# Performance work log

Hardware: AMD Instinct MI355X
Metric: run time of the kernel (lower is better)

Reference implementation:

```python
import jax, jax.numpy as jnp
import numpy as np

B, C, E = 4, 2048, 1024
H, D = 16, 64

def setup_inputs() -> dict:
    key = jax.random.key(0)
    kx, kq, kk, kv, ko = jax.random.split(key, 5)
    s = 1.0 / np.sqrt(E)
    return {
        "x": jax.random.normal(kx, (B, C, E), dtype=jnp.float32),
        "W_q": jax.random.uniform(kq, (E, H * D), jnp.float32, -s, s),
        "W_k": jax.random.uniform(kk, (E, H * D), jnp.float32, -s, s),
        "W_v": jax.random.uniform(kv, (E, H * D), jnp.float32, -s, s),
        "W_o": jax.random.uniform(ko, (H * D, E), jnp.float32, -s, s),
    }

def reference(x, W_q, W_k, W_v, W_o):
    b, c, e = x.shape
    # project and split heads: [B, H, C, D]
    q = (x @ W_q).reshape(b, c, H, D).transpose(0, 2, 1, 3)
    k = (x @ W_k).reshape(b, c, H, D).transpose(0, 2, 1, 3)
    v = (x @ W_v).reshape(b, c, H, D).transpose(0, 2, 1, 3)
    scores = jnp.einsum('bhqd,bhkd->bhqk', q, k) / jnp.sqrt(jnp.float32(D))
    causal = jnp.tril(jnp.ones((c, c), dtype=bool))
    scores = jnp.where(causal, scores, -jnp.inf)
    weights = jax.nn.softmax(scores, axis=-1)
    hidden = jnp.einsum('bhqk,bhkd->bhqd', weights, v)
    hidden = hidden.transpose(0, 2, 1, 3).reshape(b, c, H * D)
    return hidden @ W_o
```

## Files before the change

kernel.cpp:

```cpp
#include <hip/hip_runtime.h>
#include <hip/hip_bf16.h>


typedef __attribute__((ext_vector_type(8))) short short8;
typedef __attribute__((ext_vector_type(4))) float floatx4;
typedef __attribute__((ext_vector_type(4))) unsigned short ushort4v;

__device__ __forceinline__ unsigned short f2bf(float f) {
    __hip_bfloat16 h = __float2bfloat16(f);
    return __builtin_bit_cast(unsigned short, h);
}

__device__ __forceinline__ void gl2lds16(const unsigned short* g, unsigned short* l) {
    __builtin_amdgcn_global_load_lds(
        (const __attribute__((address_space(1))) unsigned int*)g,
        (__attribute__((address_space(3))) unsigned int*)l, 16, 0, 0);
}

__global__ __launch_bounds__(256) void prep_kernel(const float* __restrict__ x,
                                                   const float* __restrict__ W0,
                                                   const float* __restrict__ W1,
                                                   const float* __restrict__ W2,
                                                   const float* __restrict__ W3,
                                                   unsigned short* __restrict__ xb,
                                                   unsigned short* __restrict__ wt) {
    __shared__ float tile[64][65];
    const int id = blockIdx.x;
    if (id < 8192) {
        const int i = id * 256 + threadIdx.x;
        const float4 v = ((const float4*)x)[i];
        ushort4v o;
        o[0] = f2bf(v.x); o[1] = f2bf(v.y); o[2] = f2bf(v.z); o[3] = f2bf(v.w);
        ((ushort4v*)xb)[i] = o;
        return;
    }
    const int t2 = id - 8192;
    const int z = t2 >> 8;
    const float* src = (z == 0) ? W0 : (z == 1) ? W1 : (z == 2) ? W2 : W3;
    const float scale = (z == 0) ? 0.18033688011112042f : 1.0f;
    unsigned short* dst = wt + (size_t)z * 1048576;
    const int k0 = ((t2 >> 4) & 15) * 64, n0 = (t2 & 15) * 64;
    const int t = threadIdx.x;
    const int r = t >> 4, c4 = (t & 15) * 4;
    #pragma unroll
    for (int p = 0; p < 4; ++p) {
        const int kk = p * 16 + r;
        const float4 v = *(const float4*)&src[(size_t)(k0 + kk) * 1024 + n0 + c4];
        tile[kk][c4 + 0] = v.x; tile[kk][c4 + 1] = v.y;
        tile[kk][c4 + 2] = v.z; tile[kk][c4 + 3] = v.w;
    }
    __syncthreads();
    #pragma unroll
    for (int p = 0; p < 4; ++p) {
        const int nn = p * 16 + r;
        ushort4v o;
        #pragma unroll
        for (int j = 0; j < 4; ++j) o[j] = f2bf(tile[c4 + j][nn] * scale);
        *(ushort4v*)&dst[(size_t)(n0 + nn) * 1024 + k0 + c4] = o;
    }
}

template<int MODE, int NBLK>
__global__ __launch_bounds__(256) void gemm128(const unsigned short* __restrict__ A,
                                               const unsigned short* __restrict__ Bt,
                                               unsigned short* __restrict__ obf,
                                               float* __restrict__ ofp) {
    constexpr int Kd = 1024;
    __shared__ __align__(16) unsigned short Al[128 * 64];
    __shared__ __align__(16) unsigned short Bl[128 * 64];
    const int id = blockIdx.x;
    const int xcd = id & 7;
    const int q = id >> 3;
    const int m_blk = xcd * 8 + (q & 7);
    const int n_blk = q >> 3;
    const int m0 = m_blk * 128, n0 = n_blk * 128;

    const int tid = threadIdx.x;
    const int lane = tid & 63, w = tid >> 6;
    const int quad = lane >> 4, l15 = lane & 15;
    const int wm = (w & 1) * 64, wn = (w >> 1) * 64;
    const int srow = lane >> 3, sc = lane & 7;
    const int gc = (sc ^ srow) * 8;

    floatx4 acc[4][4];
    #pragma unroll
    for (int i = 0; i < 4; ++i)
        #pragma unroll
        for (int j = 0; j < 4; ++j) acc[i][j] = (floatx4){0.f, 0.f, 0.f, 0.f};

    for (int kt = 0; kt < Kd / 64; ++kt) {
        const int k0 = kt * 64;
        #pragma unroll
        for (int p = 0; p < 4; ++p) {
            const int row0 = w * 32 + p * 8;
            gl2lds16(&A[(size_t)(m0 + row0 + srow) * Kd + k0 + gc], &Al[row0 * 64]);
            gl2lds16(&Bt[(size_t)(n0 + row0 + srow) * Kd + k0 + gc], &Bl[row0 * 64]);
        }
        __syncthreads();
        #pragma unroll
        for (int kk = 0; kk < 2; ++kk) {
            short8 af[4], bfv[4];
            #pragma unroll
            for (int i = 0; i < 4; ++i) {
                const int row = wm + i * 16 + l15;
                af[i] = *(const short8*)&Al[row * 64 + ((kk * 4 + quad) ^ (row & 7)) * 8];
            }
            #pragma unroll
            for (int i = 0; i < 4; ++i) {
                const int row = wn + i * 16 + l15;
                bfv[i] = *(const short8*)&Bl[row * 64 + ((kk * 4 + quad) ^ (row & 7)) * 8];
            }
            #pragma unroll
            for (int i = 0; i < 4; ++i)
                #pragma unroll
                for (int j = 0; j < 4; ++j)
                    acc[i][j] = __builtin_amdgcn_mfma_f32_16x16x32_bf16(
                        af[i], bfv[j], acc[i][j], 0, 0, 0);
        }
        __syncthreads();
    }

    #pragma unroll
    for (int i = 0; i < 4; ++i) {
        if (MODE == 0 && n0 >= 2048) {
            #pragma unroll
            for (int j = 0; j < 4; ++j) {
                const int mb = m0 + wm + i * 16 + quad * 4;
                const int n = n0 + wn + j * 16 + l15;
                const int b = mb >> 11, c0 = mb & 2047;
                const int nl = n & 1023, hh = nl >> 6, d = nl & 63;
                ushort4v pv;
                #pragma unroll
                for (int r = 0; r < 4; ++r) pv[r] = f2bf(acc[i][j][r]);
                *(ushort4v*)&obf[16777216 + ((size_t)(b * 16 + hh) * 64 + d) * 2048 + c0] = pv;
            }
        } else {
            #pragma unroll
            for (int r = 0; r < 4; ++r) {
                const int m = m0 + wm + i * 16 + quad * 4 + r;
                #pragma unroll
                for (int j = 0; j < 4; ++j) {
                    const int n = n0 + wn + j * 16 + l15;
                    const float v = acc[i][j][r];
                    if (MODE == 0) {
                        const int b = m >> 11, c = m & 2047;
                        const int z = n >> 10, nl = n & 1023, hh = nl >> 6, d = nl & 63;
                        obf[(size_t)z * 8388608 +
                            ((size_t)(b * 16 + hh) * 2048 + c) * 64 + d] = f2bf(v);
                    } else {
                        ofp[(size_t)m * 1024 + n] = v;
                    }
                }
            }
        }
    }
}

__global__ __launch_bounds__(512, 8) void attn_kernel(const unsigned short* __restrict__ Q,
                                                      const unsigned short* __restrict__ K,
                                                      const unsigned short* __restrict__ Vt,
                                                      unsigned short* __restrict__ Hid) {
    __shared__ __align__(16) unsigned short Kl[64 * 64];
    __shared__ __align__(16) unsigned short Vl[64 * 64];
    __shared__ __align__(16) unsigned short Pl[8][16 * 72];
    const int id = blockIdx.x;
    const int bh = (id >> 7) * 8 + (id & 7);
    const int qt = 15 - ((id >> 3) & 15);
    const int b = bh >> 4, h = bh & 15;
    const int tid = threadIdx.x, w = tid >> 6, lane = tid & 63;
    const int quad = lane >> 4, l15 = lane & 15;
    const int sw = quad ^ (l15 & 7);
    const int srow = lane >> 3, sc = lane & 7;
    const int g8 = (sc ^ srow) * 8;
    const size_t bhs = (size_t)(b * 16 + h) * 2048 * 64;
    const unsigned short* Qb = Q + bhs;
    const unsigned short* Kb = K + bhs;
    const unsigned short* Vb = Vt + bhs;

    const int q0 = qt * 128;
    const int qw = q0 + w * 16;
    const int myq = qw + l15;
    const short8 bq0 = *(const short8*)&Qb[(size_t)myq * 64 + quad * 8];
    const short8 bq1 = *(const short8*)&Qb[(size_t)myq * 64 + 32 + quad * 8];

    floatx4 o[4];
    #pragma unroll
    for (int i = 0; i < 4; ++i) o[i] = (floatx4){0.f, 0.f, 0.f, 0.f};
    float li = 0.f;

    const int nT = (q0 + 128) >> 6;
    for (int t = 0; t < nT; ++t) {
        const int k0 = t * 64;
        {
            const int krow = w * 8 + srow;
            gl2lds16(&Kb[(size_t)(k0 + krow) * 64 + g8], &Kl[w * 512]);
            gl2lds16(&Vb[(size_t)krow * 2048 + k0 + g8], &Vl[w * 512]);
        }
        __syncthreads();
        if (k0 <= qw + 15) {
            floatx4 s[4];
            #pragma unroll
            for (int kf = 0; kf < 4; ++kf) {
                const int row = kf * 16 + l15;
                const short8 ka0 = *(const short8*)&Kl[row * 64 + sw * 8];
                const short8 ka1 = *(const short8*)&Kl[row * 64 + (sw ^ 4) * 8];
                floatx4 ss = (floatx4){0.f, 0.f, 0.f, 0.f};
                ss = __builtin_amdgcn_mfma_f32_16x16x32_bf16(ka0, bq0, ss, 0, 0, 0);
                ss = __builtin_amdgcn_mfma_f32_16x16x32_bf16(ka1, bq1, ss, 0, 0, 0);
                s[kf] = ss;
            }
            if (k0 + 63 > qw) {
                #pragma unroll
                for (int kf = 0; kf < 4; ++kf) {
                    ushort4v pw;
                    #pragma unroll
                    for (int r = 0; r < 4; ++r) {
                        const int key = k0 + kf * 16 + quad * 4 + r;
                        const float p = (key > myq) ? 0.f
                                        : __builtin_amdgcn_exp2f(s[kf][r]);
                        li += p;
                        pw[r] = f2bf(p);
                    }
                    *(ushort4v*)&Pl[w][l15 * 72 + kf * 16 + quad * 4] = pw;
                }
            } else {
                #pragma unroll
                for (int kf = 0; kf < 4; ++kf) {
                    ushort4v pw;
                    #pragma unroll
                    for (int r = 0; r < 4; ++r) {
                        const float p = __builtin_amdgcn_exp2f(s[kf][r]);
                        li += p;
                        pw[r] = f2bf(p);
                    }
                    *(ushort4v*)&Pl[w][l15 * 72 + kf * 16 + quad * 4] = pw;
                }
            }
            __threadfence_block();
            const short8 pb0 = *(const short8*)&Pl[w][l15 * 72 + quad * 8];
            const short8 pb1 = *(const short8*)&Pl[w][l15 * 72 + 32 + quad * 8];
            #pragma unroll
            for (int nt = 0; nt < 4; ++nt) {
                const int row = nt * 16 + l15;
                const short8 va0 = *(const short8*)&Vl[row * 64 + sw * 8];
                const short8 va1 = *(const short8*)&Vl[row * 64 + (sw ^ 4) * 8];
                floatx4 oo = o[nt];
                oo = __builtin_amdgcn_mfma_f32_16x16x32_bf16(va0, pb0, oo, 0, 0, 0);
                oo = __builtin_amdgcn_mfma_f32_16x16x32_bf16(va1, pb1, oo, 0, 0, 0);
                o[nt] = oo;
            }
        }
        __syncthreads();
    }

    li += __shfl_xor(li, 16, 64);
    li += __shfl_xor(li, 32, 64);
    const float inv = 1.f / li;
    #pragma unroll
    for (int nt = 0; nt < 4; ++nt) {
        ushort4v ov;
        #pragma unroll
        for (int r = 0; r < 4; ++r) ov[r] = f2bf(o[nt][r] * inv);
        *(ushort4v*)&Hid[((size_t)b * 2048 + myq) * 1024 + h * 64 + nt * 16 + quad * 4] = ov;
    }
}

extern "C" void kernel_launch(void* const* d_in, const int* in_sizes, int n_in,
                              void* d_out, int out_size, void* d_ws, size_t ws_size,
                              hipStream_t stream) {
    const float* x  = (const float*)d_in[0];
    const float* Wq = (const float*)d_in[1];
    const float* Wk = (const float*)d_in[2];
    const float* Wv = (const float*)d_in[3];
    const float* Wo = (const float*)d_in[4];
    float* out = (float*)d_out;
    unsigned short* ws = (unsigned short*)d_ws;

    const size_t XB  = 0;
    const size_t WQT = 8388608;
    const size_t QO  = 12582912;
    const size_t HO  = 37748736;

    prep_kernel<<<9216, 256, 0, stream>>>(x, Wq, Wk, Wv, Wo, ws + XB, ws + WQT);

    gemm128<0, 24><<<1536, 256, 0, stream>>>(ws + XB, ws + WQT, ws + QO, nullptr);
    attn_kernel<<<1024, 512, 0, stream>>>(ws + QO, ws + QO + 8388608,
                                          ws + QO + 16777216, ws + HO);
    gemm128<1, 8><<<512, 256, 0, stream>>>(ws + HO, ws + WQT + 3145728, nullptr, out);
}
```

Before: 262.7 us.

## Double-buffer K/V tiles and pair causal query tiles per attention block

The attention kernel now double-buffers K and V tiles in shared memory, so the next tile's global-to-LDS load is issued before the current tile is computed, and one barrier per iteration is removed. Each block also handles two query tiles, xq and 15-xq, so every block gets the same causal work and the grid is halved to 512 blocks. The aim is to hide load latency and balance work across blocks. In exchange, LDS use doubles and the occupancy hint in launch_bounds is dropped, which may lower occupancy, and the smaller grid may leave compute units idle.

```diff
diff --git a/kernel.cpp b/kernel.cpp
--- a/kernel.cpp
+++ b/kernel.cpp
@@ -156,112 +156,121 @@
     }
 }
 
-__global__ __launch_bounds__(512, 8) void attn_kernel(const unsigned short* __restrict__ Q,
-                                                      const unsigned short* __restrict__ K,
-                                                      const unsigned short* __restrict__ Vt,
-                                                      unsigned short* __restrict__ Hid) {
-    __shared__ __align__(16) unsigned short Kl[64 * 64];
-    __shared__ __align__(16) unsigned short Vl[64 * 64];
+__global__ __launch_bounds__(512) void attn_kernel(const unsigned short* __restrict__ Q,
+                                                   const unsigned short* __restrict__ K,
+                                                   const unsigned short* __restrict__ Vt,
+                                                   unsigned short* __restrict__ Hid) {
+    __shared__ __align__(16) unsigned short Kl[2][64 * 64];
+    __shared__ __align__(16) unsigned short Vl[2][64 * 64];
     __shared__ __align__(16) unsigned short Pl[8][16 * 72];
     const int id = blockIdx.x;
-    const int bh = (id >> 7) * 8 + (id & 7);
-    const int qt = 15 - ((id >> 3) & 15);
+    const int bh = (id >> 6) * 8 + (id & 7);
+    const int xq = (id >> 3) & 7;
     const int b = bh >> 4, h = bh & 15;
     const int tid = threadIdx.x, w = tid >> 6, lane = tid & 63;
     const int quad = lane >> 4, l15 = lane & 15;
     const int sw = quad ^ (l15 & 7);
     const int srow = lane >> 3, sc = lane & 7;
     const int g8 = (sc ^ srow) * 8;
+    const int krow = w * 8 + srow;
     const size_t bhs = (size_t)(b * 16 + h) * 2048 * 64;
     const unsigned short* Qb = Q + bhs;
     const unsigned short* Kb = K + bhs;
     const unsigned short* Vb = Vt + bhs;
 
-    const int q0 = qt * 128;
-    const int qw = q0 + w * 16;
-    const int myq = qw + l15;
-    const short8 bq0 = *(const short8*)&Qb[(size_t)myq * 64 + quad * 8];
-    const short8 bq1 = *(const short8*)&Qb[(size_t)myq * 64 + 32 + quad * 8];
-
-    floatx4 o[4];
-    #pragma unroll
-    for (int i = 0; i < 4; ++i) o[i] = (floatx4){0.f, 0.f, 0.f, 0.f};
-    float li = 0.f;
-
-    const int nT = (q0 + 128) >> 6;
-    for (int t = 0; t < nT; ++t) {
-        const int k0 = t * 64;
-        {
-            const int krow = w * 8 + srow;
-            gl2lds16(&Kb[(size_t)(k0 + krow) * 64 + g8], &Kl[w * 512]);
-            gl2lds16(&Vb[(size_t)krow * 2048 + k0 + g8], &Vl[w * 512]);
-        }
+    #pragma unroll
+    for (int pass = 0; pass < 2; ++pass) {
+        const int qt = pass ? (15 - xq) : xq;
+        const int q0 = qt * 128;
+        const int qw = q0 + w * 16;
+        const int myq = qw + l15;
+        const short8 bq0 = *(const short8*)&Qb[(size_t)myq * 64 + quad * 8];
+        const short8 bq1 = *(const short8*)&Qb[(size_t)myq * 64 + 32 + quad * 8];
+
+        floatx4 o[4];
+        #pragma unroll
+        for (int i = 0; i < 4; ++i) o[i] = (floatx4){0.f, 0.f, 0.f, 0.f};
+        float li = 0.f;
+
+        const int nT = (q0 + 128) >> 6;
         __syncthreads();
-        if (k0 <= qw + 15) {
-            floatx4 s[4];
-            #pragma unroll
-            for (int kf = 0; kf < 4; ++kf) {
-                const int row = kf * 16 + l15;
-                const short8 ka0 = *(const short8*)&Kl[row * 64 + sw * 8];
-                const short8 ka1 = *(const short8*)&Kl[row * 64 + (sw ^ 4) * 8];
-                floatx4 ss = (floatx4){0.f, 0.f, 0.f, 0.f};
-                ss = __builtin_amdgcn_mfma_f32_16x16x32_bf16(ka0, bq0, ss, 0, 0, 0);
-                ss = __builtin_amdgcn_mfma_f32_16x16x32_bf16(ka1, bq1, ss, 0, 0, 0);
-                s[kf] = ss;
-            }
-            if (k0 + 63 > qw) {
+        gl2lds16(&Kb[(size_t)krow * 64 + g8], &Kl[0][w * 512]);
+        gl2lds16(&Vb[(size_t)krow * 2048 + g8], &Vl[0][w * 512]);
+
+        for (int t = 0; t < nT; ++t) {
+            const int k0 = t * 64;
+            const int cb = t & 1;
+            __syncthreads();
+            if (t + 1 < nT) {
+                const int kn = k0 + 64;
+                gl2lds16(&Kb[(size_t)(kn + krow) * 64 + g8], &Kl[cb ^ 1][w * 512]);
+                gl2lds16(&Vb[(size_t)krow * 2048 + kn + g8], &Vl[cb ^ 1][w * 512]);
+            }
+            if (k0 <= qw + 15) {
+                floatx4 s[4];
                 #pragma unroll
                 for (int kf = 0; kf < 4; ++kf) {
-                    ushort4v pw;
+                    const int row = kf * 16 + l15;
+                    const short8 ka0 = *(const short8*)&Kl[cb][row * 64 + sw * 8];
+                    const short8 ka1 = *(const short8*)&Kl[cb][row * 64 + (sw ^ 4) * 8];
+                    floatx4 ss = (floatx4){0.f, 0.f, 0.f, 0.f};
+                    ss = __builtin_amdgcn_mfma_f32_16x16x32_bf16(ka0, bq0, ss, 0, 0, 0);
+                    ss = __builtin_amdgcn_mfma_f32_16x16x32_bf16(ka1, bq1, ss, 0, 0, 0);
+                    s[kf] = ss;
+                }
+                if (k0 + 63 > qw) {
                     #pragma unroll
-                    for (int r = 0; r < 4; ++r) {
-                        const int key = k0 + kf * 16 + quad * 4 + r;
-                        const float p = (key > myq) ? 0.f
-                                        : __builtin_amdgcn_exp2f(s[kf][r]);
-                        li += p;
-                        pw[r] = f2bf(p);
+                    for (int kf = 0; kf < 4; ++kf) {
+                        ushort4v pw;
+                        #pragma unroll
+                        for (int r = 0; r < 4; ++r) {
+                            const int key = k0 + kf * 16 + quad * 4 + r;
+                            const float p = (key > myq) ? 0.f
+                                            : __builtin_amdgcn_exp2f(s[kf][r]);
+                            li += p;
+                            pw[r] = f2bf(p);
+                        }
+                        *(ushort4v*)&Pl[w][l15 * 72 + kf * 16 + quad * 4] = pw;
                     }
-                    *(ushort4v*)&Pl[w][l15 * 72 + kf * 16 + quad * 4] = pw;
-                }
-            } else {
-                #pragma unroll
-                for (int kf = 0; kf < 4; ++kf) {
-                    ushort4v pw;
+                } else {
                     #pragma unroll
-                    for (int r = 0; r < 4; ++r) {
-                        const float p = __builtin_amdgcn_exp2f(s[kf][r]);
-                        li += p;
-                        pw[r] = f2bf(p);
+                    for (int kf = 0; kf < 4; ++kf) {
+                        ushort4v pw;
+                        #pragma unroll
+                        for (int r = 0; r < 4; ++r) {
+                            const float p = __builtin_amdgcn_exp2f(s[kf][r]);
+                            li += p;
+                            pw[r] = f2bf(p);
+                        }
+                        *(ushort4v*)&Pl[w][l15 * 72 + kf * 16 + quad * 4] = pw;
                     }
-                    *(ushort4v*)&Pl[w][l15 * 72 + kf * 16 + quad * 4] = pw;
-                }
-            }
-            __threadfence_block();
-            const short8 pb0 = *(const short8*)&Pl[w][l15 * 72 + quad * 8];
-            const short8 pb1 = *(const short8*)&Pl[w][l15 * 72 + 32 + quad * 8];
-            #pragma unroll
-            for (int nt = 0; nt < 4; ++nt) {
-                const int row = nt * 16 + l15;
-                const short8 va0 = *(const short8*)&Vl[row * 64 + sw * 8];
-                const short8 va1 = *(const short8*)&Vl[row * 64 + (sw ^ 4) * 8];
-                floatx4 oo = o[nt];
-                oo = __builtin_amdgcn_mfma_f32_16x16x32_bf16(va0, pb0, oo, 0, 0, 0);
-                oo = __builtin_amdgcn_mfma_f32_16x16x32_bf16(va1, pb1, oo, 0, 0, 0);
-                o[nt] = oo;
-            }
-        }
-        __syncthreads();
-    }
-
-    li += __shfl_xor(li, 16, 64);
-    li += __shfl_xor(li, 32, 64);
-    const float inv = 1.f / li;
-    #pragma unroll
-    for (int nt = 0; nt < 4; ++nt) {
-        ushort4v ov;
-        #pragma unroll
-        for (int r = 0; r < 4; ++r) ov[r] = f2bf(o[nt][r] * inv);
-        *(ushort4v*)&Hid[((size_t)b * 2048 + myq) * 1024 + h * 64 + nt * 16 + quad * 4] = ov;
+                }
+                __threadfence_block();
+                const short8 pb0 = *(const short8*)&Pl[w][l15 * 72 + quad * 8];
+                const short8 pb1 = *(const short8*)&Pl[w][l15 * 72 + 32 + quad * 8];
+                #pragma unroll
+                for (int nt = 0; nt < 4; ++nt) {
+                    const int row = nt * 16 + l15;
+                    const short8 va0 = *(const short8*)&Vl[cb][row * 64 + sw * 8];
+                    const short8 va1 = *(const short8*)&Vl[cb][row * 64 + (sw ^ 4) * 8];
+                    floatx4 oo = o[nt];
+                    oo = __builtin_amdgcn_mfma_f32_16x16x32_bf16(va0, pb0, oo, 0, 0, 0);
+                    oo = __builtin_amdgcn_mfma_f32_16x16x32_bf16(va1, pb1, oo, 0, 0, 0);
+                    o[nt] = oo;
+                }
+            }
+        }
+
+        li += __shfl_xor(li, 16, 64);
+        li += __shfl_xor(li, 32, 64);
+        const float inv = 1.f / li;
+        #pragma unroll
+        for (int nt = 0; nt < 4; ++nt) {
+            ushort4v ov;
+            #pragma unroll
+            for (int r = 0; r < 4; ++r) ov[r] = f2bf(o[nt][r] * inv);
+            *(ushort4v*)&Hid[((size_t)b * 2048 + myq) * 1024 + h * 64 + nt * 16 + quad * 4] = ov;
+        }
     }
 }
 
@@ -284,7 +293,7 @@
     prep_kernel<<<9216, 256, 0, stream>>>(x, Wq, Wk, Wv, Wo, ws + XB, ws + WQT);
 
     gemm128<0, 24><<<1536, 256, 0, stream>>>(ws + XB, ws + WQT, ws + QO, nullptr);
-    attn_kernel<<<1024, 512, 0, stream>>>(ws + QO, ws + QO + 8388608,
-                                          ws + QO + 16777216, ws + HO);
+    attn_kernel<<<512, 512, 0, stream>>>(ws + QO, ws + QO + 8388608,
+                                         ws + QO + 16777216, ws + HO);
     gemm128<1, 8><<<512, 256, 0, stream>>>(ws + HO, ws + WQT + 3145728, nullptr, out);
 }
```

New measurement: 232.9 us. -11.3%, faster.
